# Optimization experiments

Hardware: AMD Instinct MI355X
Metric: run time of the kernel (lower is better)

## Reference

```python
import jax, jax.numpy as jnp
import numpy as np

B, S, D, H = 1, 2048, 4096, 32
HD = D // H
THETA = 10000.0
IN_SCALE = 0.1   # input_scale buffer
Q_SCALE = 0.1    # q_proj_scale buffer
K_SCALE = 0.1    # k_proj_scale buffer
V_SCALE = 0.1    # v_proj_scale buffer
OUT_SCALE = 0.1  # out_input_scale buffer


def _fake_q(x, scale, lo, hi):
    # round-to-int + clamp, kept in float (faithful to int8 fake-quant)
    return jnp.clip(jnp.round(x / scale), lo, hi)


def _w4a8_linear(x, qw, w_scale, in_scale):
    # int8 fake-quantized activation x int4-valued weight, dequant output
    qx = _fake_q(x, in_scale, -128, 127)
    return jnp.einsum('bsd,od->bso', qx, qw) * (in_scale * w_scale)


def _rope_tables(position_ids):
    inv_freq = 1.0 / (THETA ** (jnp.arange(0, HD, 2, dtype=jnp.float32) / HD))
    ang = position_ids.astype(jnp.float32)[..., None] * inv_freq  # [B,S,HD/2]
    emb = jnp.concatenate([ang, ang], axis=-1)                     # [B,S,HD]
    return jnp.cos(emb)[:, None], jnp.sin(emb)[:, None]            # [B,1,S,HD]


def _rotate_half(x):
    return jnp.concatenate([-x[..., HD // 2:], x[..., :HD // 2]], axis=-1)


def setup_inputs() -> dict:
    key = jax.random.key(0)
    ks = jax.random.split(key, 9)
    hidden_states = jax.random.normal(ks[0], (B, S, D), jnp.float32)
    def int4_w(k):
        return jnp.round(jax.random.uniform(k, (D, D), jnp.float32, -8.0, 7.0))
    def ch_scale(k):
        return jax.random.uniform(k, (D,), jnp.float32, 0.01, 0.03)
    wq, wk, wv, wo = int4_w(ks[1]), int4_w(ks[2]), int4_w(ks[3]), int4_w(ks[4])
    sq_w, sk_w, sv_w, so_w = ch_scale(ks[5]), ch_scale(ks[6]), ch_scale(ks[7]), ch_scale(ks[8])
    position_ids = jnp.arange(S, dtype=jnp.int32)[None, :]
    causal = jnp.tril(jnp.ones((S, S), dtype=bool))
    attention_mask = jnp.where(causal, 0.0, -1e9).astype(jnp.float32)[None, None]
    return dict(hidden_states=hidden_states, wq=wq, wk=wk, wv=wv, wo=wo,
                sq_w=sq_w, sk_w=sk_w, sv_w=sv_w, so_w=so_w,
                attention_mask=attention_mask, position_ids=position_ids)


def reference(hidden_states, wq, wk, wv, wo, sq_w, sk_w, sv_w, so_w,
              attention_mask, position_ids):
    # W4A8 dequant projections
    q = _w4a8_linear(hidden_states, wq, sq_w, IN_SCALE)
    k = _w4a8_linear(hidden_states, wk, sk_w, IN_SCALE)
    v = _w4a8_linear(hidden_states, wv, sv_w, IN_SCALE)
    q = q.reshape(B, S, H, HD).transpose(0, 2, 1, 3)  # [B,H,S,HD]
    k = k.reshape(B, S, H, HD).transpose(0, 2, 1, 3)
    v = v.reshape(B, S, H, HD).transpose(0, 2, 1, 3)
    # RoPE
    cos, sin = _rope_tables(position_ids)
    q = q * cos + _rotate_half(q) * sin
    k = k * cos + _rotate_half(k) * sin
    # int8 fake-quant of q/k/v, then dequant before matmuls
    q = _fake_q(q, Q_SCALE, -128, 127)
    k = _fake_q(k, K_SCALE, -128, 127)
    v = _fake_q(v, V_SCALE, -128, 127)
    scores = jnp.einsum('bhqd,bhkd->bhqk', q * Q_SCALE, k * K_SCALE) / np.sqrt(HD)
    scores = scores + attention_mask
    attn = jax.nn.softmax(scores.astype(jnp.float32), axis=-1)
    out = jnp.einsum('bhqk,bhkd->bhqd', attn, v * V_SCALE)
    out = out.transpose(0, 2, 1, 3).reshape(B, S, D)
    # o_proj input re-quantized to int8 with out_input_scale (clamp -127..127)
    out_q = _fake_q(out, OUT_SCALE, -127, 127)
    attn_output = jnp.einsum('bsd,od->bso', out_q, wo) * (OUT_SCALE * so_w)
    return attn_output
```

## Files before the change

### kernel.cpp

```cpp
#include <hip/hip_runtime.h>
#include <math.h>
#include <stdint.h>

#define S_LEN 2048
#define D_DIM 4096
#define NHEAD 32
#define HDIM  128

typedef int      v4i __attribute__((ext_vector_type(4)));
typedef float    v4f __attribute__((ext_vector_type(4)));
typedef _Float16 v8h __attribute__((ext_vector_type(8)));

__device__ __forceinline__ float quant128(float x) {
  return fminf(fmaxf(rintf(x / 0.1f), -128.f), 127.f);
}
__device__ __forceinline__ void gl_lds16(const void* g, void* l) {
  __builtin_amdgcn_global_load_lds(
      (const __attribute__((address_space(1))) void*)g,
      (__attribute__((address_space(3))) void*)l, 16, 0, 0);
}

__global__ __launch_bounds__(256) void quant_hidden_k(const float* __restrict__ in,
                                                      int8_t* __restrict__ out) {
  const int idx = blockIdx.x * 256 + threadIdx.x;
  const float4 v = ((const float4*)in)[idx];
  const int q0 = (int)quant128(v.x), q1 = (int)quant128(v.y);
  const int q2 = (int)quant128(v.z), q3 = (int)quant128(v.w);
  ((int*)out)[idx] = (q0 & 0xff) | ((q1 & 0xff) << 8) | ((q2 & 0xff) << 16) | ((q3 & 0xff) << 24);
}

__global__ __launch_bounds__(256) void wconv3_k(const float* __restrict__ a,
                                                const float* __restrict__ b,
                                                const float* __restrict__ c,
                                                int8_t* __restrict__ out) {
  const int which = blockIdx.x >> 14;
  const int sub = blockIdx.x & 16383;
  const float* src = (which == 0) ? a : (which == 1) ? b : c;
  const int idx = sub * 256 + threadIdx.x;
  const float4 v = ((const float4*)src)[idx];
  const int q0 = __float2int_rn(v.x), q1 = __float2int_rn(v.y);
  const int q2 = __float2int_rn(v.z), q3 = __float2int_rn(v.w);
  ((int*)out)[(size_t)which * 4194304 + idx] =
      (q0 & 0xff) | ((q1 & 0xff) << 8) | ((q2 & 0xff) << 16) | ((q3 & 0xff) << 24);
}

__global__ __launch_bounds__(256) void wconv_k(const float* __restrict__ in,
                                               int8_t* __restrict__ out) {
  const int idx = blockIdx.x * 256 + threadIdx.x;
  const float4 v = ((const float4*)in)[idx];
  const int q0 = __float2int_rn(v.x), q1 = __float2int_rn(v.y);
  const int q2 = __float2int_rn(v.z), q3 = __float2int_rn(v.w);
  ((int*)out)[idx] = (q0 & 0xff) | ((q1 & 0xff) << 8) | ((q2 & 0xff) << 16) | ((q3 & 0xff) << 24);
}

__global__ __launch_bounds__(256) void rope_tab_k(const int* __restrict__ pos,
                                                  float* __restrict__ ct,
                                                  float* __restrict__ st) {
  const int idx = blockIdx.x * 256 + threadIdx.x;
  const int s = idx >> 6, j = idx & 63;
  const float inv = exp2f((float)j * -0.20762050593046016f);
  const float a = (float)pos[s] * inv;
  float si, c;
  sincosf(a, &si, &c);
  ct[idx] = c;
  st[idx] = si;
}

template <int OMODE>
__global__ __launch_bounds__(256) void gemm_i8(
    const int8_t* __restrict__ A8, const int8_t* __restrict__ W8,
    const float* __restrict__ wsc, const float* __restrict__ ctab,
    const float* __restrict__ stab, void* __restrict__ outp) {
  __shared__ __align__(16) int8_t Als[16384];
  __shared__ __align__(16) int8_t Bls[16384];
  const int t = threadIdx.x;
  const int w = t >> 6, lane = t & 63, g = lane >> 4, l15 = lane & 15;
  const int G = blockIdx.x;
  const int within = G & 15, g16 = G >> 4;
  const int bn = ((g16 & 7) * 4 + (within & 3)) * 128;
  const int bm = ((g16 >> 3) * 4 + (within >> 2)) * 128;

  const int srow = lane >> 3;
  const int schunk = ((lane & 7) ^ srow) * 16;
  const int8_t* sA[4];
  const int8_t* sB[4];
  int8_t* dA[4];
  int8_t* dB[4];
#pragma unroll
  for (int i = 0; i < 4; ++i) {
    const int row = w * 32 + i * 8 + srow;
    sA[i] = A8 + (size_t)(bm + row) * D_DIM + schunk;
    sB[i] = W8 + (size_t)(bn + row) * D_DIM + schunk;
    dA[i] = Als + w * 4096 + i * 1024;
    dB[i] = Bls + w * 4096 + i * 1024;
  }

  v4i acc[8][2];
#pragma unroll
  for (int i = 0; i < 8; ++i) {
    acc[i][0] = (v4i){0, 0, 0, 0};
    acc[i][1] = (v4i){0, 0, 0, 0};
  }

  for (int k0 = 0; k0 < D_DIM; k0 += 128) {
#pragma unroll
    for (int i = 0; i < 4; ++i) {
      gl_lds16(sA[i] + k0, dA[i]);
      gl_lds16(sB[i] + k0, dB[i]);
    }
    __syncthreads();
#pragma unroll
    for (int kk = 0; kk < 2; ++kk) {
      const int coff = (((kk << 2) | g) ^ (l15 & 7)) * 16;
      const v4i bf0 = *(const v4i*)(Bls + (w * 16 + l15) * 128 + coff);
      const v4i bf1 = *(const v4i*)(Bls + (w * 16 + 64 + l15) * 128 + coff);
#pragma unroll
      for (int mi = 0; mi < 8; ++mi) {
        const v4i af = *(const v4i*)(Als + (mi * 16 + l15) * 128 + coff);
        acc[mi][0] = __builtin_amdgcn_mfma_i32_16x16x64_i8(af, bf0, acc[mi][0], 0, 0, 0);
        acc[mi][1] = __builtin_amdgcn_mfma_i32_16x16x64_i8(af, bf1, acc[mi][1], 0, 0, 0);
      }
    }
    __syncthreads();
  }

  if (OMODE == 0 || OMODE == 1) {
    const int jcol = w * 16 + l15;
    const float sc0 = 0.1f * wsc[bn + jcol];
    const float sc1 = 0.1f * wsc[bn + jcol + 64];
    int8_t* dst = (int8_t*)outp;
#pragma unroll
    for (int mi = 0; mi < 8; ++mi) {
#pragma unroll
      for (int r = 0; r < 4; ++r) {
        const int s = bm + mi * 16 + g * 4 + r;
        const float c = ctab[s * 64 + jcol];
        const float si = stab[s * 64 + jcol];
        const float x1 = (float)acc[mi][0][r] * sc0;
        const float x2 = (float)acc[mi][1][r] * sc1;
        dst[(size_t)s * D_DIM + bn + jcol] = (int8_t)quant128(x1 * c - x2 * si);
        dst[(size_t)s * D_DIM + bn + jcol + 64] = (int8_t)quant128(x2 * c + x1 * si);
      }
    }
  } else if (OMODE == 2) {
    _Float16* dst = (_Float16*)outp;
#pragma unroll
    for (int jt = 0; jt < 2; ++jt) {
      const int col = bn + w * 16 + jt * 64 + l15;
      const float scv = 0.1f * wsc[col];
#pragma unroll
      for (int mi = 0; mi < 8; ++mi) {
#pragma unroll
        for (int r = 0; r < 4; ++r) {
          const int s = bm + mi * 16 + g * 4 + r;
          dst[(size_t)col * S_LEN + s] = (_Float16)quant128((float)acc[mi][jt][r] * scv);
        }
      }
    }
  } else {
    float* dst = (float*)outp;
#pragma unroll
    for (int jt = 0; jt < 2; ++jt) {
      const int col = bn + w * 16 + jt * 64 + l15;
      const float scv = 0.1f * wsc[col];
#pragma unroll
      for (int mi = 0; mi < 8; ++mi) {
#pragma unroll
        for (int r = 0; r < 4; ++r) {
          const int s = bm + mi * 16 + g * 4 + r;
          dst[(size_t)s * D_DIM + col] = (float)acc[mi][jt][r] * scv;
        }
      }
    }
  }
}

__global__ __launch_bounds__(256, 3) void attn_v5(
    const int8_t* __restrict__ q8, const int8_t* __restrict__ k8,
    const _Float16* __restrict__ vT, int8_t* __restrict__ o8) {
  __shared__ __align__(16) int8_t Kls[2][8192];
  __shared__ __align__(16) int8_t Vls[2][16384];
  const int j = 31 - blockIdx.x;
  const int h = blockIdx.y;
  const int t = threadIdx.x;
  const int w = t >> 6, lane = t & 63, g = lane >> 4, l15 = lane & 15;
  const int T = j + 1;
  const int q0 = (4 * j + w) * 16;
  const int q_lane = q0 + l15;
  const float SSCALE = 8.838834764831845e-4f;
  const v8h vones = {(_Float16)1, (_Float16)1, (_Float16)1, (_Float16)1,
                     (_Float16)1, (_Float16)1, (_Float16)1, (_Float16)1};

  int k_src[2], v_src[4], kv_dst[4];
#pragma unroll
  for (int i = 0; i < 2; ++i) {
    const int lin = i * 256 + t;
    const int s = lin >> 3;
    const int cs = (lin & 7) ^ (s & 7);
    const int key = ((s >> 5) & 1) * 32 + ((s >> 3) & 1) * 16 +
                    ((s >> 2) & 1) * 8 + ((s >> 4) & 1) * 4 + (s & 3);
    k_src[i] = key * D_DIM + cs * 16;
  }
#pragma unroll
  for (int i = 0; i < 4; ++i) {
    const int lin = i * 256 + t;
    const int d = lin >> 3;
    const int cs = (lin & 7) ^ (d & 7);
    v_src[i] = d * S_LEN + cs * 8;
    kv_dst[i] = lin * 16;
  }
  const int8_t* kbg = k8 + (size_t)h * HDIM;
  const _Float16* vbg = vT + (size_t)h * HDIM * S_LEN;

  auto stage = [&](int kt, int b) {
    const int8_t* ks = kbg + (size_t)kt * (64 * D_DIM);
    const _Float16* vs = vbg + kt * 64;
#pragma unroll
    for (int i = 0; i < 2; ++i) gl_lds16(ks + k_src[i], Kls[b] + kv_dst[i]);
#pragma unroll
    for (int i = 0; i < 4; ++i) gl_lds16(vs + v_src[i], Vls[b] + kv_dst[i]);
  };

  const v4i qa0 = *(const v4i*)(q8 + (size_t)q_lane * D_DIM + h * HDIM + g * 16);
  const v4i qa1 = *(const v4i*)(q8 + (size_t)q_lane * D_DIM + h * HDIM + 64 + g * 16);

  v4f o[8];
#pragma unroll
  for (int n = 0; n < 8; ++n) o[n] = (v4f){0.f, 0.f, 0.f, 0.f};
  v4f lacc = (v4f){0.f, 0.f, 0.f, 0.f};
  float m_i = -INFINITY;

  stage(0, 0);

  for (int kt = 0; kt < T; ++kt) {
    const int b = kt & 1;
    __syncthreads();
    if (kt + 1 < T) stage(kt + 1, b ^ 1);

    const int ksw = (l15 & 7);
    float sc[4][4];
#pragma unroll
    for (int nt = 0; nt < 4; ++nt) {
      const int8_t* kr = Kls[b] + (nt * 16 + l15) * 128;
      const v4i kb0 = *(const v4i*)(kr + ((g ^ ksw) * 16));
      const v4i kb1 = *(const v4i*)(kr + (((4 + g) ^ ksw) * 16));
      v4i c = (v4i){0, 0, 0, 0};
      c = __builtin_amdgcn_mfma_i32_16x16x64_i8(kb0, qa0, c, 0, 0, 0);
      c = __builtin_amdgcn_mfma_i32_16x16x64_i8(kb1, qa1, c, 0, 0, 0);
#pragma unroll
      for (int r = 0; r < 4; ++r) {
        float s = (float)c[r] * SSCALE;
        if (kt == T - 1) {
          const int key = kt * 64 + ((nt >> 1) << 5) + ((g >> 1) << 4) +
                          ((g & 1) << 3) + ((nt & 1) << 2) + r;
          if (key > q_lane) s = -1.0e30f;
        }
        sc[nt][r] = s;
      }
    }
    float mx = fmaxf(fmaxf(fmaxf(sc[0][0], sc[0][1]), fmaxf(sc[0][2], sc[0][3])),
                     fmaxf(fmaxf(sc[1][0], sc[1][1]), fmaxf(sc[1][2], sc[1][3])));
    mx = fmaxf(mx, fmaxf(fmaxf(fmaxf(sc[2][0], sc[2][1]), fmaxf(sc[2][2], sc[2][3])),
                         fmaxf(fmaxf(sc[3][0], sc[3][1]), fmaxf(sc[3][2], sc[3][3]))));
    mx = fmaxf(mx, __shfl_xor(mx, 16));
    mx = fmaxf(mx, __shfl_xor(mx, 32));
    const float mnew = fmaxf(m_i, mx);
    const float alpha = __expf(m_i - mnew);
    m_i = mnew;

    float p[4][4];
#pragma unroll
    for (int nt = 0; nt < 4; ++nt)
#pragma unroll
      for (int r = 0; r < 4; ++r) p[nt][r] = __expf(sc[nt][r] - m_i);

    v8h ph0, ph1;
#pragma unroll
    for (int e = 0; e < 8; ++e) {
      ph0[e] = (_Float16)p[e >> 2][e & 3];
      ph1[e] = (_Float16)p[2 + (e >> 2)][e & 3];
    }
    float a_r[4];
#pragma unroll
    for (int r = 0; r < 4; ++r)
      a_r[r] = __shfl(alpha, (lane & 48) | (g * 4 + r));
#pragma unroll
    for (int n = 0; n < 8; ++n)
#pragma unroll
      for (int r = 0; r < 4; ++r) o[n][r] *= a_r[r];
#pragma unroll
    for (int r = 0; r < 4; ++r) lacc[r] *= a_r[r];

    __builtin_amdgcn_s_setprio(1);
    lacc = __builtin_amdgcn_mfma_f32_16x16x32_f16(ph0, vones, lacc, 0, 0, 0);
    lacc = __builtin_amdgcn_mfma_f32_16x16x32_f16(ph1, vones, lacc, 0, 0, 0);
#pragma unroll
    for (int nt = 0; nt < 8; ++nt) {
      const int8_t* vr = Vls[b] + (nt * 16 + l15) * 128;
      const v8h v0 = *(const v8h*)(vr + ((g ^ ksw) * 16));
      const v8h v1 = *(const v8h*)(vr + (((4 + g) ^ ksw) * 16));
      o[nt] = __builtin_amdgcn_mfma_f32_16x16x32_f16(ph0, v0, o[nt], 0, 0, 0);
      o[nt] = __builtin_amdgcn_mfma_f32_16x16x32_f16(ph1, v1, o[nt], 0, 0, 0);
    }
    __builtin_amdgcn_s_setprio(0);
  }

#pragma unroll
  for (int r = 0; r < 4; ++r) {
    const float rL = 1.0f / lacc[r];
    const size_t row = (size_t)(q0 + g * 4 + r) * D_DIM + h * HDIM;
#pragma unroll
    for (int nt = 0; nt < 8; ++nt) {
      const int q = (int)fminf(fmaxf(rintf(o[nt][r] * rL), -127.f), 127.f);
      o8[row + nt * 16 + l15] = (int8_t)q;
    }
  }
}

extern "C" void kernel_launch(void* const* d_in, const int* in_sizes, int n_in,
                              void* d_out, int out_size, void* d_ws, size_t ws_size,
                              hipStream_t stream) {
  (void)in_sizes; (void)n_in; (void)out_size; (void)ws_size;
  const float* hidden = (const float*)d_in[0];
  const float* wq = (const float*)d_in[1];
  const float* wk = (const float*)d_in[2];
  const float* wv = (const float*)d_in[3];
  const float* wo = (const float*)d_in[4];
  const float* sq = (const float*)d_in[5];
  const float* sk = (const float*)d_in[6];
  const float* sv = (const float*)d_in[7];
  const float* so = (const float*)d_in[8];
  const int* pos = (const int*)d_in[10];
  float* out = (float*)d_out;

  char* ws = (char*)d_ws;
  int8_t* h8 = (int8_t*)ws;
  int8_t* q8 = (int8_t*)(ws + (8ull << 20));
  int8_t* k8 = (int8_t*)(ws + (16ull << 20));
  _Float16* vT = (_Float16*)(ws + (24ull << 20));
  int8_t* w8a = (int8_t*)(ws + (40ull << 20));
  int8_t* w8b = (int8_t*)(ws + (56ull << 20));
  int8_t* w8c = (int8_t*)(ws + (72ull << 20));
  float* ctab = (float*)(ws + (88ull << 20));
  float* stab = (float*)(ws + (88ull << 20) + (512ull << 10));
  int8_t* o8 = h8;

  hipLaunchKernelGGL(rope_tab_k, dim3(512), dim3(256), 0, stream, pos, ctab, stab);
  hipLaunchKernelGGL(quant_hidden_k, dim3(8192), dim3(256), 0, stream, hidden, h8);
  hipLaunchKernelGGL(wconv3_k, dim3(49152), dim3(256), 0, stream, wq, wk, wv, w8a);

  const dim3 gg(512), gb(256);
  hipLaunchKernelGGL((gemm_i8<0>), gg, gb, 0, stream, h8, w8a, sq, ctab, stab, (void*)q8);
  hipLaunchKernelGGL((gemm_i8<1>), gg, gb, 0, stream, h8, w8b, sk, ctab, stab, (void*)k8);
  hipLaunchKernelGGL((gemm_i8<2>), gg, gb, 0, stream, h8, w8c, sv, ctab, stab, (void*)vT);
  hipLaunchKernelGGL(wconv_k, dim3(16384), dim3(256), 0, stream, wo, w8a);
  hipLaunchKernelGGL(attn_v5, dim3(32, 32), dim3(256), 0, stream, q8, k8, vT, o8);
  hipLaunchKernelGGL((gemm_i8<3>), gg, gb, 0, stream, o8, w8a, so, ctab, stab, (void*)out);
}
```

Baseline: 575.3 us.

## Fuse QKV GEMMs into one launch with triple-buffered 128x256 int8 tiles

Replaces the per-projection int8 GEMM with a 512-thread kernel using 128x256 tiles and a three-stage LDS ring buffer. Global-to-LDS loads for tile k+2 are issued while MFMAs run on tile k, using explicit vmcnt waits and setprio around the MFMA bursts. The Q, K and V projections now run as a single launch over the concatenated weight matrix, with the output mode chosen per column segment. This is meant to hide load latency, raise reuse per tile and cut launch count. In exchange it needs 144KB of LDS at one block per CU, which lowers occupancy and makes the code depend on the LDS capacity.

Result: faster. 518.9 us (-9.8%).

```diff
diff --git a/kernel.cpp b/kernel.cpp
--- a/kernel.cpp
+++ b/kernel.cpp
@@ -66,110 +66,151 @@
   st[idx] = si;
 }
 
-template <int OMODE>
-__global__ __launch_bounds__(256) void gemm_i8(
+template <int MODE>
+__global__ __launch_bounds__(512, 1) void gemm8p(
     const int8_t* __restrict__ A8, const int8_t* __restrict__ W8,
-    const float* __restrict__ wsc, const float* __restrict__ ctab,
-    const float* __restrict__ stab, void* __restrict__ outp) {
-  __shared__ __align__(16) int8_t Als[16384];
-  __shared__ __align__(16) int8_t Bls[16384];
+    const float* __restrict__ s0, const float* __restrict__ s1,
+    const float* __restrict__ s2, const float* __restrict__ ctab,
+    const float* __restrict__ stab, void* __restrict__ out0,
+    void* __restrict__ out1, void* __restrict__ out2) {
+  __shared__ __align__(16) int8_t LS[3 * 16384 + 3 * 32768];
+  int8_t* const Abase = LS;
+  int8_t* const Bbase = LS + 49152;
+
   const int t = threadIdx.x;
   const int w = t >> 6, lane = t & 63, g = lane >> 4, l15 = lane & 15;
+  const int wm = w >> 2, wn = w & 3;
+
   const int G = blockIdx.x;
   const int within = G & 15, g16 = G >> 4;
-  const int bn = ((g16 & 7) * 4 + (within & 3)) * 128;
-  const int bm = ((g16 >> 3) * 4 + (within >> 2)) * 128;
-
-  const int srow = lane >> 3;
-  const int schunk = ((lane & 7) ^ srow) * 16;
-  const int8_t* sA[4];
-  const int8_t* sB[4];
-  int8_t* dA[4];
-  int8_t* dB[4];
-#pragma unroll
-  for (int i = 0; i < 4; ++i) {
-    const int row = w * 32 + i * 8 + srow;
-    sA[i] = A8 + (size_t)(bm + row) * D_DIM + schunk;
-    sB[i] = W8 + (size_t)(bn + row) * D_DIM + schunk;
-    dA[i] = Als + w * 4096 + i * 1024;
-    dB[i] = Bls + w * 4096 + i * 1024;
-  }
-
-  v4i acc[8][2];
-#pragma unroll
-  for (int i = 0; i < 8; ++i) {
-    acc[i][0] = (v4i){0, 0, 0, 0};
-    acc[i][1] = (v4i){0, 0, 0, 0};
-  }
-
-  for (int k0 = 0; k0 < D_DIM; k0 += 128) {
-#pragma unroll
-    for (int i = 0; i < 4; ++i) {
-      gl_lds16(sA[i] + k0, dA[i]);
-      gl_lds16(sB[i] + k0, dB[i]);
-    }
-    __syncthreads();
-#pragma unroll
-    for (int kk = 0; kk < 2; ++kk) {
-      const int coff = (((kk << 2) | g) ^ (l15 & 7)) * 16;
-      const v4i bf0 = *(const v4i*)(Bls + (w * 16 + l15) * 128 + coff);
-      const v4i bf1 = *(const v4i*)(Bls + (w * 16 + 64 + l15) * 128 + coff);
-#pragma unroll
-      for (int mi = 0; mi < 8; ++mi) {
-        const v4i af = *(const v4i*)(Als + (mi * 16 + l15) * 128 + coff);
-        acc[mi][0] = __builtin_amdgcn_mfma_i32_16x16x64_i8(af, bf0, acc[mi][0], 0, 0, 0);
-        acc[mi][1] = __builtin_amdgcn_mfma_i32_16x16x64_i8(af, bf1, acc[mi][1], 0, 0, 0);
-      }
-    }
-    __syncthreads();
-  }
-
-  if (OMODE == 0 || OMODE == 1) {
-    const int jcol = w * 16 + l15;
-    const float sc0 = 0.1f * wsc[bn + jcol];
-    const float sc1 = 0.1f * wsc[bn + jcol + 64];
-    int8_t* dst = (int8_t*)outp;
-#pragma unroll
-    for (int mi = 0; mi < 8; ++mi) {
-#pragma unroll
-      for (int r = 0; r < 4; ++r) {
-        const int s = bm + mi * 16 + g * 4 + r;
-        const float c = ctab[s * 64 + jcol];
-        const float si = stab[s * 64 + jcol];
-        const float x1 = (float)acc[mi][0][r] * sc0;
-        const float x2 = (float)acc[mi][1][r] * sc1;
-        dst[(size_t)s * D_DIM + bn + jcol] = (int8_t)quant128(x1 * c - x2 * si);
-        dst[(size_t)s * D_DIM + bn + jcol + 64] = (int8_t)quant128(x2 * c + x1 * si);
-      }
-    }
-  } else if (OMODE == 2) {
-    _Float16* dst = (_Float16*)outp;
-#pragma unroll
-    for (int jt = 0; jt < 2; ++jt) {
-      const int col = bn + w * 16 + jt * 64 + l15;
-      const float scv = 0.1f * wsc[col];
-#pragma unroll
-      for (int mi = 0; mi < 8; ++mi) {
-#pragma unroll
-        for (int r = 0; r < 4; ++r) {
-          const int s = bm + mi * 16 + g * 4 + r;
-          dst[(size_t)col * S_LEN + s] = (_Float16)quant128((float)acc[mi][jt][r] * scv);
+  const int bm = ((g16 & 3) * 4 + (within >> 2)) * 128;
+  const int bn = ((g16 >> 2) * 4 + (within & 3)) * 256;
+
+  const int rowo = lane >> 3;
+  const int schunk = ((lane & 7) ^ rowo) * 16;
+  const int8_t* srcA[2];
+  const int8_t* srcB[4];
+#pragma unroll
+  for (int i = 0; i < 2; ++i)
+    srcA[i] = A8 + (size_t)(bm + w * 16 + i * 8 + rowo) * D_DIM + schunk;
+#pragma unroll
+  for (int i = 0; i < 4; ++i)
+    srcB[i] = W8 + (size_t)(bn + w * 32 + i * 8 + rowo) * D_DIM + schunk;
+
+#define STAGE(KT, BI)                                                       \
+  {                                                                         \
+    const int kof_ = (KT) * 128;                                            \
+    int8_t* Ad_ = Abase + (BI) * 16384 + w * 2048;                          \
+    int8_t* Bd_ = Bbase + (BI) * 32768 + w * 4096;                          \
+    _Pragma("unroll") for (int i_ = 0; i_ < 2; ++i_)                        \
+        gl_lds16(srcA[i_] + kof_, Ad_ + i_ * 1024);                         \
+    _Pragma("unroll") for (int i_ = 0; i_ < 4; ++i_)                        \
+        gl_lds16(srcB[i_] + kof_, Bd_ + i_ * 1024);                         \
+  }
+
+  const int nc0 = (wn & 1) * 32 + (wn >> 1) * 128;
+
+  v4i acc[4][4];
+#pragma unroll
+  for (int mi = 0; mi < 4; ++mi)
+#pragma unroll
+    for (int ni = 0; ni < 4; ++ni) acc[mi][ni] = (v4i){0, 0, 0, 0};
+
+  STAGE(0, 0)
+  STAGE(1, 1)
+
+  for (int t3 = 0; t3 < 33; t3 += 3) {
+#pragma unroll
+    for (int u = 0; u < 3; ++u) {
+      const int kt = t3 + u;
+      if (kt < 32) {
+        if (kt + 1 < 32)
+          asm volatile("s_waitcnt vmcnt(6)" ::: "memory");
+        else
+          asm volatile("s_waitcnt vmcnt(0)" ::: "memory");
+        __builtin_amdgcn_s_barrier();
+        if (kt + 2 < 32) STAGE(kt + 2, ((u + 2) % 3))
+        const int8_t* Ab = Abase + u * 16384;
+        const int8_t* Bb = Bbase + u * 32768;
+#pragma unroll
+        for (int kk = 0; kk < 2; ++kk) {
+          const int coff = (((kk << 2) | g) ^ (l15 & 7)) * 16;
+          v4i bf[4], af[4];
+#pragma unroll
+          for (int ni = 0; ni < 4; ++ni) {
+            const int nrow = nc0 + (ni & 1) * 16 + (ni >> 1) * 64 + l15;
+            bf[ni] = *(const v4i*)(Bb + nrow * 128 + coff);
+          }
+#pragma unroll
+          for (int mi = 0; mi < 4; ++mi)
+            af[mi] = *(const v4i*)(Ab + (wm * 64 + mi * 16 + l15) * 128 + coff);
+          __builtin_amdgcn_s_setprio(1);
+#pragma unroll
+          for (int mi = 0; mi < 4; ++mi)
+#pragma unroll
+            for (int ni = 0; ni < 4; ++ni)
+              acc[mi][ni] =
+                  __builtin_amdgcn_mfma_i32_16x16x64_i8(af[mi], bf[ni], acc[mi][ni], 0, 0, 0);
+          __builtin_amdgcn_s_setprio(0);
         }
       }
     }
+  }
+#undef STAGE
+
+  const int srow0 = bm + wm * 64;
+  if (MODE == 1) {
+    float* dst = (float*)out0;
+#pragma unroll
+    for (int ni = 0; ni < 4; ++ni) {
+      const int col = bn + nc0 + (ni & 1) * 16 + (ni >> 1) * 64 + l15;
+      const float sc = 0.1f * s0[col];
+#pragma unroll
+      for (int mi = 0; mi < 4; ++mi)
+#pragma unroll
+        for (int r = 0; r < 4; ++r)
+          dst[(size_t)(srow0 + mi * 16 + g * 4 + r) * D_DIM + col] =
+              (float)acc[mi][ni][r] * sc;
+    }
   } else {
-    float* dst = (float*)outp;
-#pragma unroll
-    for (int jt = 0; jt < 2; ++jt) {
-      const int col = bn + w * 16 + jt * 64 + l15;
-      const float scv = 0.1f * wsc[col];
-#pragma unroll
-      for (int mi = 0; mi < 8; ++mi) {
-#pragma unroll
-        for (int r = 0; r < 4; ++r) {
-          const int s = bm + mi * 16 + g * 4 + r;
-          dst[(size_t)s * D_DIM + col] = (float)acc[mi][jt][r] * scv;
-        }
+    const int seg = bn >> 12;
+    const int bcol = bn & 4095;
+    if (seg == 2) {
+      _Float16* dst = (_Float16*)out2;
+#pragma unroll
+      for (int ni = 0; ni < 4; ++ni) {
+        const int col = bcol + nc0 + (ni & 1) * 16 + (ni >> 1) * 64 + l15;
+        const float scv = 0.1f * s2[col];
+#pragma unroll
+        for (int mi = 0; mi < 4; ++mi)
+#pragma unroll
+          for (int r = 0; r < 4; ++r) {
+            const int s = srow0 + mi * 16 + g * 4 + r;
+            dst[(size_t)col * S_LEN + s] = (_Float16)quant128((float)acc[mi][ni][r] * scv);
+          }
+      }
+    } else {
+      const float* wsc = seg ? s1 : s0;
+      int8_t* dst = seg ? (int8_t*)out1 : (int8_t*)out0;
+      const int hb = bcol + (wn >> 1) * 128;
+#pragma unroll
+      for (int ni = 0; ni < 2; ++ni) {
+        const int dlo = (wn & 1) * 32 + ni * 16 + l15;
+        const int clo = hb + dlo;
+        const float sc0 = 0.1f * wsc[clo];
+        const float sc1 = 0.1f * wsc[clo + 64];
+#pragma unroll
+        for (int mi = 0; mi < 4; ++mi)
+#pragma unroll
+          for (int r = 0; r < 4; ++r) {
+            const int s = srow0 + mi * 16 + g * 4 + r;
+            const float c = ctab[s * 64 + dlo];
+            const float si = stab[s * 64 + dlo];
+            const float x1 = (float)acc[mi][ni][r] * sc0;
+            const float x2 = (float)acc[mi][ni + 2][r] * sc1;
+            dst[(size_t)s * D_DIM + clo] = (int8_t)quant128(x1 * c - x2 * si);
+            dst[(size_t)s * D_DIM + clo + 64] = (int8_t)quant128(x2 * c + x1 * si);
+          }
       }
     }
   }
@@ -349,11 +390,10 @@
   hipLaunchKernelGGL(quant_hidden_k, dim3(8192), dim3(256), 0, stream, hidden, h8);
   hipLaunchKernelGGL(wconv3_k, dim3(49152), dim3(256), 0, stream, wq, wk, wv, w8a);
 
-  const dim3 gg(512), gb(256);
-  hipLaunchKernelGGL((gemm_i8<0>), gg, gb, 0, stream, h8, w8a, sq, ctab, stab, (void*)q8);
-  hipLaunchKernelGGL((gemm_i8<1>), gg, gb, 0, stream, h8, w8b, sk, ctab, stab, (void*)k8);
-  hipLaunchKernelGGL((gemm_i8<2>), gg, gb, 0, stream, h8, w8c, sv, ctab, stab, (void*)vT);
+  hipLaunchKernelGGL((gemm8p<0>), dim3(768), dim3(512), 0, stream, h8, w8a,
+                     sq, sk, sv, ctab, stab, (void*)q8, (void*)k8, (void*)vT);
   hipLaunchKernelGGL(wconv_k, dim3(16384), dim3(256), 0, stream, wo, w8a);
   hipLaunchKernelGGL(attn_v5, dim3(32, 32), dim3(256), 0, stream, q8, k8, vT, o8);
-  hipLaunchKernelGGL((gemm_i8<3>), gg, gb, 0, stream, o8, w8a, so, ctab, stab, (void*)out);
-}
+  hipLaunchKernelGGL((gemm8p<1>), dim3(256), dim3(512), 0, stream, o8, w8a,
+                     so, so, so, ctab, stab, (void*)out, (void*)out, (void*)out);
+}
```
